# Kernel tuning notes

Measured on AMD Instinct MI355X. Metric: run time of the kernel, lower is better.

The kernel has to match this reference:

```python
import jax, jax.numpy as jnp
import numpy as np

N_NODES = 100000
N_EDGES = 800000
D_IN = 128      # input_dim (node feature dim)
D_HID = 128     # output_dim (MLP hidden dim)


def setup_inputs() -> dict:
    key = jax.random.key(0)
    ks = jax.random.split(key, 7)
    node_emb = jax.random.normal(ks[0], (N_NODES, D_IN), dtype=jnp.float32)
    src = jax.random.randint(ks[1], (N_EDGES,), 0, N_NODES, dtype=jnp.int64)
    dst = jax.random.randint(ks[2], (N_EDGES,), 0, N_NODES, dtype=jnp.int64)
    W1 = jax.random.normal(ks[3], (2 * D_IN, D_HID), dtype=jnp.float32) / np.sqrt(2 * D_IN)
    b1 = jnp.zeros((D_HID,), dtype=jnp.float32)
    W2 = jax.random.normal(ks[4], (D_HID, 1), dtype=jnp.float32) / np.sqrt(D_HID)
    b2 = jnp.zeros((1,), dtype=jnp.float32)
    u_gate = jax.random.uniform(ks[5], (N_EDGES, 1), dtype=jnp.float32)  # torch.rand noise for gumbel gate
    u_bern = jax.random.uniform(ks[6], (N_EDGES,), dtype=jnp.float32)    # uniform noise for RelaxedBernoulli.rsample
    return {"node_emb": node_emb, "src": src, "dst": dst,
            "W1": W1, "b1": b1, "W2": W2, "b2": b2,
            "u_gate": u_gate, "u_bern": u_bern}


def reference(node_emb, src, dst, W1, b1, W2, b2, u_gate, u_bern):
    BIAS = 1e-4          # bias in forward
    TEMP_GATE = 1.0      # temperature in forward
    TEMP_BERN = 0.9      # temperature passed to build_prob_neighbourhood

    # edge gather + concat: [E, 2*D_IN]
    edge_emb = jnp.concatenate([node_emb[src], node_emb[dst]], axis=1)
    # 2-layer per-edge MLP -> logits [E, 1]
    h = jax.nn.relu(edge_emb @ W1 + b1)
    edge_logits = h @ W2 + b2

    # gumbel-sigmoid gate: eps in (BIAS, 1-BIAS]
    eps = (BIAS - (1.0 - BIAS)) * u_gate + (1.0 - BIAS)
    gate_inputs = (jnp.log(eps) - jnp.log1p(-eps) + edge_logits) / TEMP_GATE
    edge_weight = jax.nn.sigmoid(gate_inputs).squeeze(-1)  # [E]

    # build_prob_neighbourhood: RelaxedBernoulli(temperature=0.9, probs=clamped).rsample()
    attention = jnp.clip(edge_weight, 0.01, 0.99)
    bern_logits = jnp.log(attention) - jnp.log1p(-attention)
    u = jnp.clip(u_bern, 1e-7, 1.0 - 1e-7)
    w = jax.nn.sigmoid((bern_logits + jnp.log(u) - jnp.log1p(-u)) / TEMP_BERN)

    # mask = (w > 0).detach().float(); w = w*mask + 0*(1-mask)
    mask = jax.lax.stop_gradient((w > 0.0).astype(w.dtype))
    return w * mask
```

## Files before the change

### kernel.cpp

```cpp
#include <hip/hip_runtime.h>
#include <hip/hip_bf16.h>
#include <cstdint>

#define D  128
#define NT 256

typedef __attribute__((ext_vector_type(8))) short bf16x8;
typedef __attribute__((ext_vector_type(4))) float f32x4;

__device__ __forceinline__ unsigned int packbf(float lo, float hi) {
    const unsigned int ulo = __float_as_uint(lo) + 0x8000u;
    const unsigned int uhi = __float_as_uint(hi) + 0x8000u;
    return __builtin_amdgcn_perm(uhi, ulo, 0x07060302);
}

__global__ __launch_bounds__(256, 2) void node_mlp_mfma(
    const float* __restrict__ x, const float* __restrict__ W1,
    unsigned short* __restrict__ T, int N)
{
    const int lane = threadIdx.x & 63;
    const int wid  = (blockIdx.x * blockDim.x + threadIdx.x) >> 6;
    const int half = wid & 1;
    const int strip = wid >> 1;
    const int lr = lane & 15;
    const int lg = lane >> 4;

    const int NCH = (N + 15) >> 4;

    bf16x8 wf[8][4];
    #pragma unroll
    for (int cg = 0; cg < 8; ++cg) {
        #pragma unroll
        for (int ks = 0; ks < 4; ++ks) {
            const int k0 = (half ? 128 : 0) + 32 * ks + 8 * lg;
            const float* wp = W1 + (size_t)k0 * D + cg * 16 + lr;
            float l0 = wp[0*D], l1 = wp[1*D], l2 = wp[2*D], l3 = wp[3*D];
            float l4 = wp[4*D], l5 = wp[5*D], l6 = wp[6*D], l7 = wp[7*D];
            uint4 u;
            u.x = packbf(l0, l1); u.y = packbf(l2, l3);
            u.z = packbf(l4, l5); u.w = packbf(l6, l7);
            wf[cg][ks] = __builtin_bit_cast(bf16x8, u);
        }
    }

    int c = strip;
    if (c >= NCH) return;

    size_t row = (size_t)(c * 16 + lr);
    if (row > (size_t)(N - 1)) row = (size_t)(N - 1);
    const float4* pf = reinterpret_cast<const float4*>(x + row * D + 8 * lg);
    float4 r0 = pf[0],  r1 = pf[1],  r2 = pf[8],  r3 = pf[9];
    float4 r4 = pf[16], r5 = pf[17], r6 = pf[24], r7 = pf[25];

    while (c < NCH) {
        bf16x8 xf[4];
        {
            uint4 u;
            u.x = packbf(r0.x, r0.y); u.y = packbf(r0.z, r0.w);
            u.z = packbf(r1.x, r1.y); u.w = packbf(r1.z, r1.w);
            xf[0] = __builtin_bit_cast(bf16x8, u);
            u.x = packbf(r2.x, r2.y); u.y = packbf(r2.z, r2.w);
            u.z = packbf(r3.x, r3.y); u.w = packbf(r3.z, r3.w);
            xf[1] = __builtin_bit_cast(bf16x8, u);
            u.x = packbf(r4.x, r4.y); u.y = packbf(r4.z, r4.w);
            u.z = packbf(r5.x, r5.y); u.w = packbf(r5.z, r5.w);
            xf[2] = __builtin_bit_cast(bf16x8, u);
            u.x = packbf(r6.x, r6.y); u.y = packbf(r6.z, r6.w);
            u.z = packbf(r7.x, r7.y); u.w = packbf(r7.z, r7.w);
            xf[3] = __builtin_bit_cast(bf16x8, u);
        }

        const int cn = c + 1024;
        {
            size_t row2 = (size_t)(cn * 16 + lr);
            if (row2 > (size_t)(N - 1)) row2 = (size_t)(N - 1);
            pf = reinterpret_cast<const float4*>(x + row2 * D + 8 * lg);
        }
        float4 t0 = pf[0],  t1 = pf[1],  t2 = pf[8],  t3 = pf[9];
        float4 t4 = pf[16], t5 = pf[17], t6 = pf[24], t7 = pf[25];

        f32x4 acc[8];
        #pragma unroll
        for (int cg = 0; cg < 8; ++cg) acc[cg] = (f32x4){0.f, 0.f, 0.f, 0.f};
        #pragma unroll
        for (int ks = 0; ks < 4; ++ks) {
            #pragma unroll
            for (int cg = 0; cg < 8; ++cg) {
                acc[cg] = __builtin_amdgcn_mfma_f32_16x16x32_bf16(
                    wf[cg][ks], xf[ks], acc[cg], 0, 0, 0);
            }
        }

        const int node = c * 16 + lr;
        if (node < N) {
            unsigned short* orow = T + (size_t)node * NT + half * 128 + lg * 4;
            #pragma unroll
            for (int cg = 0; cg < 8; ++cg) {
                uint2 o;
                o.x = packbf(acc[cg][0], acc[cg][1]);
                o.y = packbf(acc[cg][2], acc[cg][3]);
                *reinterpret_cast<uint2*>(orow + cg * 16) = o;
            }
        }

        r0 = t0; r1 = t1; r2 = t2; r3 = t3;
        r4 = t4; r5 = t5; r6 = t6; r7 = t7;
        c = cn;
    }
}

__device__ __forceinline__ float acc_pair(uint32_t wa, uint32_t wb,
                                          float blo, float bhi,
                                          float w2lo, float w2hi, float p) {
    const float alo = __uint_as_float(wa << 16);
    const float ahi = __uint_as_float(wa & 0xffff0000u);
    const float clo = __uint_as_float(wb << 16);
    const float chi = __uint_as_float(wb & 0xffff0000u);
    const float h0 = fmaxf(alo + clo + blo, 0.f);
    const float h1 = fmaxf(ahi + chi + bhi, 0.f);
    p = fmaf(h0, w2lo, p);
    p = fmaf(h1, w2hi, p);
    return p;
}

__global__ __launch_bounds__(256) void edge_kernel(
    const unsigned short* __restrict__ T,
    const int* __restrict__ src, const int* __restrict__ dst,
    const float* __restrict__ b1, const float* __restrict__ W2,
    const float* __restrict__ b2,
    const float* __restrict__ u_gate, const float* __restrict__ u_bern,
    float* __restrict__ out, int E)
{
    const int gid = blockIdx.x * blockDim.x + threadIdx.x;
    const int e = gid >> 3;
    if (e >= E) return;
    const int sub = threadIdx.x & 7;

    const int s = src[e];
    const int d = dst[e];

    const uint4* Ap = reinterpret_cast<const uint4*>(T + (size_t)s * NT + sub * 16);
    const uint4* Bp = reinterpret_cast<const uint4*>(T + (size_t)d * NT + 128 + sub * 16);
    const float4* Bv = reinterpret_cast<const float4*>(b1 + sub * 16);
    const float4* Wv = reinterpret_cast<const float4*>(W2 + sub * 16);

    const uint4 a0 = Ap[0], a1 = Ap[1];
    const uint4 c0 = Bp[0], c1 = Bp[1];
    const float4 bb0 = Bv[0], bb1 = Bv[1], bb2 = Bv[2], bb3 = Bv[3];
    const float4 w0 = Wv[0], w1 = Wv[1], w2 = Wv[2], w3 = Wv[3];

    float p = 0.f;
    p = acc_pair(a0.x, c0.x, bb0.x, bb0.y, w0.x, w0.y, p);
    p = acc_pair(a0.y, c0.y, bb0.z, bb0.w, w0.z, w0.w, p);
    p = acc_pair(a0.z, c0.z, bb1.x, bb1.y, w1.x, w1.y, p);
    p = acc_pair(a0.w, c0.w, bb1.z, bb1.w, w1.z, w1.w, p);
    p = acc_pair(a1.x, c1.x, bb2.x, bb2.y, w2.x, w2.y, p);
    p = acc_pair(a1.y, c1.y, bb2.z, bb2.w, w2.z, w2.w, p);
    p = acc_pair(a1.z, c1.z, bb3.x, bb3.y, w3.x, w3.y, p);
    p = acc_pair(a1.w, c1.w, bb3.z, bb3.w, w3.z, w3.w, p);

    p += __shfl_xor(p, 1, 64);
    p += __shfl_xor(p, 2, 64);
    p += __shfl_xor(p, 4, 64);

    if (sub == 0) {
        const float logit = p + b2[0];

        const float ug  = u_gate[e];
        const float eps = fmaf(-0.9998f, ug, 0.9999f);
        const float g   = logf(eps) - log1pf(-eps) + logit;
        const float ew  = 1.f / (1.f + expf(-g));

        const float att = fminf(fmaxf(ew, 0.01f), 0.99f);
        const float bl  = logf(att) - log1pf(-att);
        const float ub  = fminf(fmaxf(u_bern[e], 1e-7f), 1.f - 1e-7f);
        const float arg = (bl + logf(ub) - log1pf(-ub)) * (1.0f / 0.9f);
        const float wv  = 1.f / (1.f + expf(-arg));

        out[e] = wv;
    }
}

extern "C" void kernel_launch(void* const* d_in, const int* in_sizes, int n_in,
                              void* d_out, int out_size, void* d_ws, size_t ws_size,
                              hipStream_t stream)
{
    const float* node_emb = (const float*)d_in[0];
    const int*   src      = (const int*)d_in[1];
    const int*   dst      = (const int*)d_in[2];
    const float* W1       = (const float*)d_in[3];
    const float* b1       = (const float*)d_in[4];
    const float* W2       = (const float*)d_in[5];
    const float* b2       = (const float*)d_in[6];
    const float* u_gate   = (const float*)d_in[7];
    const float* u_bern   = (const float*)d_in[8];
    float* out = (float*)d_out;

    const int N = in_sizes[0] / D;
    const int E = in_sizes[1];

    unsigned short* T = (unsigned short*)d_ws;

    node_mlp_mfma<<<512, 256, 0, stream>>>(node_emb, W1, T, N);

    const long long dotThreads = (long long)E * 8;
    const int blocksE = (int)((dotThreads + 255) / 256);
    edge_kernel<<<blocksE, 256, 0, stream>>>(T, src, dst, b1, W2, b2,
                                             u_gate, u_bern, out, E);
}
```

Baseline: 200.3 us.

## Pre-pack W1 into LDS, compute both halves per wave, persistent prefetching edge kernel

```diff
diff --git a/kernel.cpp b/kernel.cpp
--- a/kernel.cpp
+++ b/kernel.cpp
@@ -14,45 +14,57 @@
     return __builtin_amdgcn_perm(uhi, ulo, 0x07060302);
 }
 
-__global__ __launch_bounds__(256, 2) void node_mlp_mfma(
-    const float* __restrict__ x, const float* __restrict__ W1,
+__global__ __launch_bounds__(256) void pack_w1(
+    const float* __restrict__ W1, unsigned short* __restrict__ Wp)
+{
+    const int t = blockIdx.x * 256 + threadIdx.x;
+    if (t >= 4096) return;
+    const int lane = t & 63;
+    const int fc = t >> 6;
+    const int cg = fc >> 2, ks = fc & 3;
+    const int lr = lane & 15, lg = lane >> 4;
+    const int half = cg >> 3;
+    const int col = (cg & 7) * 16 + lr;
+    const int krow = half * 128 + ks * 32 + lg * 8;
+    const float* wp = W1 + (size_t)krow * D + col;
+    uint4 u;
+    u.x = packbf(wp[0 * D], wp[1 * D]);
+    u.y = packbf(wp[2 * D], wp[3 * D]);
+    u.z = packbf(wp[4 * D], wp[5 * D]);
+    u.w = packbf(wp[6 * D], wp[7 * D]);
+    reinterpret_cast<uint4*>(Wp)[t] = u;
+}
+
+__global__ __launch_bounds__(512, 4) void node_mlp_mfma(
+    const float* __restrict__ x, const unsigned short* __restrict__ Wp,
     unsigned short* __restrict__ T, int N)
 {
+    __shared__ uint4 ldsW[4096];
+
+    {
+        const uint4* s = reinterpret_cast<const uint4*>(Wp);
+        #pragma unroll
+        for (int i = 0; i < 8; ++i)
+            ldsW[threadIdx.x + i * 512] = s[threadIdx.x + i * 512];
+    }
+    __syncthreads();
+
     const int lane = threadIdx.x & 63;
-    const int wid  = (blockIdx.x * blockDim.x + threadIdx.x) >> 6;
-    const int half = wid & 1;
-    const int strip = wid >> 1;
-    const int lr = lane & 15;
-    const int lg = lane >> 4;
-
+    const int wib  = threadIdx.x >> 6;
+    const int wid  = blockIdx.x * 8 + wib;
+    const int nW   = gridDim.x * 8;
+    const int lr = lane & 15, lg = lane >> 4;
     const int NCH = (N + 15) >> 4;
 
-    bf16x8 wf[8][4];
-    #pragma unroll
-    for (int cg = 0; cg < 8; ++cg) {
-        #pragma unroll
-        for (int ks = 0; ks < 4; ++ks) {
-            const int k0 = (half ? 128 : 0) + 32 * ks + 8 * lg;
-            const float* wp = W1 + (size_t)k0 * D + cg * 16 + lr;
-            float l0 = wp[0*D], l1 = wp[1*D], l2 = wp[2*D], l3 = wp[3*D];
-            float l4 = wp[4*D], l5 = wp[5*D], l6 = wp[6*D], l7 = wp[7*D];
-            uint4 u;
-            u.x = packbf(l0, l1); u.y = packbf(l2, l3);
-            u.z = packbf(l4, l5); u.w = packbf(l6, l7);
-            wf[cg][ks] = __builtin_bit_cast(bf16x8, u);
-        }
-    }
-
-    int c = strip;
-    if (c >= NCH) return;
-
-    size_t row = (size_t)(c * 16 + lr);
-    if (row > (size_t)(N - 1)) row = (size_t)(N - 1);
-    const float4* pf = reinterpret_cast<const float4*>(x + row * D + 8 * lg);
-    float4 r0 = pf[0],  r1 = pf[1],  r2 = pf[8],  r3 = pf[9];
-    float4 r4 = pf[16], r5 = pf[17], r6 = pf[24], r7 = pf[25];
-
-    while (c < NCH) {
+    const uint4* fragBase = ldsW + lane;
+
+    for (int c = wid; c < NCH; c += nW) {
+        int row = c * 16 + lr;
+        if (row >= N) row = N - 1;
+        const float4* pf = reinterpret_cast<const float4*>(x + (size_t)row * D + 8 * lg);
+        const float4 r0 = pf[0],  r1 = pf[1],  r2 = pf[8],  r3 = pf[9];
+        const float4 r4 = pf[16], r5 = pf[17], r6 = pf[24], r7 = pf[25];
+
         bf16x8 xf[4];
         {
             uint4 u;
@@ -70,42 +82,30 @@
             xf[3] = __builtin_bit_cast(bf16x8, u);
         }
 
-        const int cn = c + 1024;
-        {
-            size_t row2 = (size_t)(cn * 16 + lr);
-            if (row2 > (size_t)(N - 1)) row2 = (size_t)(N - 1);
-            pf = reinterpret_cast<const float4*>(x + row2 * D + 8 * lg);
-        }
-        float4 t0 = pf[0],  t1 = pf[1],  t2 = pf[8],  t3 = pf[9];
-        float4 t4 = pf[16], t5 = pf[17], t6 = pf[24], t7 = pf[25];
-
-        f32x4 acc[8];
+        f32x4 acc[16];
         #pragma unroll
-        for (int cg = 0; cg < 8; ++cg) acc[cg] = (f32x4){0.f, 0.f, 0.f, 0.f};
+        for (int cg = 0; cg < 16; ++cg) acc[cg] = (f32x4){0.f, 0.f, 0.f, 0.f};
+
         #pragma unroll
         for (int ks = 0; ks < 4; ++ks) {
             #pragma unroll
-            for (int cg = 0; cg < 8; ++cg) {
-                acc[cg] = __builtin_amdgcn_mfma_f32_16x16x32_bf16(
-                    wf[cg][ks], xf[ks], acc[cg], 0, 0, 0);
+            for (int cg = 0; cg < 16; ++cg) {
+                const bf16x8 wf = __builtin_bit_cast(bf16x8, fragBase[(cg * 4 + ks) * 64]);
+                acc[cg] = __builtin_amdgcn_mfma_f32_16x16x32_bf16(wf, xf[ks], acc[cg], 0, 0, 0);
             }
         }
 
         const int node = c * 16 + lr;
         if (node < N) {
-            unsigned short* orow = T + (size_t)node * NT + half * 128 + lg * 4;
+            unsigned short* orow = T + (size_t)node * NT + lg * 4;
             #pragma unroll
-            for (int cg = 0; cg < 8; ++cg) {
+            for (int cg = 0; cg < 16; ++cg) {
                 uint2 o;
                 o.x = packbf(acc[cg][0], acc[cg][1]);
                 o.y = packbf(acc[cg][2], acc[cg][3]);
                 *reinterpret_cast<uint2*>(orow + cg * 16) = o;
             }
         }
-
-        r0 = t0; r1 = t1; r2 = t2; r3 = t3;
-        r4 = t4; r5 = t5; r6 = t6; r7 = t7;
-        c = cn;
     }
 }
 
@@ -131,53 +131,68 @@
     const float* __restrict__ u_gate, const float* __restrict__ u_bern,
     float* __restrict__ out, int E)
 {
-    const int gid = blockIdx.x * blockDim.x + threadIdx.x;
-    const int e = gid >> 3;
+    const int sub = threadIdx.x & 7;
+    const int g0 = (blockIdx.x * blockDim.x + threadIdx.x) >> 3;
+    const int gstride = (gridDim.x * blockDim.x) >> 3;
+
+    const float4* Bv = reinterpret_cast<const float4*>(b1 + sub * 16);
+    const float4* Wv = reinterpret_cast<const float4*>(W2 + sub * 16);
+    const float4 bb0 = Bv[0], bb1 = Bv[1], bb2 = Bv[2], bb3 = Bv[3];
+    const float4 w0 = Wv[0], w1 = Wv[1], w2 = Wv[2], w3 = Wv[3];
+    const float b2v = b2[0];
+
+    int e = g0;
     if (e >= E) return;
-    const int sub = threadIdx.x & 7;
-
-    const int s = src[e];
-    const int d = dst[e];
-
+
+    int s = src[e], d = dst[e];
     const uint4* Ap = reinterpret_cast<const uint4*>(T + (size_t)s * NT + sub * 16);
     const uint4* Bp = reinterpret_cast<const uint4*>(T + (size_t)d * NT + 128 + sub * 16);
-    const float4* Bv = reinterpret_cast<const float4*>(b1 + sub * 16);
-    const float4* Wv = reinterpret_cast<const float4*>(W2 + sub * 16);
-
-    const uint4 a0 = Ap[0], a1 = Ap[1];
-    const uint4 c0 = Bp[0], c1 = Bp[1];
-    const float4 bb0 = Bv[0], bb1 = Bv[1], bb2 = Bv[2], bb3 = Bv[3];
-    const float4 w0 = Wv[0], w1 = Wv[1], w2 = Wv[2], w3 = Wv[3];
-
-    float p = 0.f;
-    p = acc_pair(a0.x, c0.x, bb0.x, bb0.y, w0.x, w0.y, p);
-    p = acc_pair(a0.y, c0.y, bb0.z, bb0.w, w0.z, w0.w, p);
-    p = acc_pair(a0.z, c0.z, bb1.x, bb1.y, w1.x, w1.y, p);
-    p = acc_pair(a0.w, c0.w, bb1.z, bb1.w, w1.z, w1.w, p);
-    p = acc_pair(a1.x, c1.x, bb2.x, bb2.y, w2.x, w2.y, p);
-    p = acc_pair(a1.y, c1.y, bb2.z, bb2.w, w2.z, w2.w, p);
-    p = acc_pair(a1.z, c1.z, bb3.x, bb3.y, w3.x, w3.y, p);
-    p = acc_pair(a1.w, c1.w, bb3.z, bb3.w, w3.z, w3.w, p);
-
-    p += __shfl_xor(p, 1, 64);
-    p += __shfl_xor(p, 2, 64);
-    p += __shfl_xor(p, 4, 64);
-
-    if (sub == 0) {
-        const float logit = p + b2[0];
-
-        const float ug  = u_gate[e];
-        const float eps = fmaf(-0.9998f, ug, 0.9999f);
-        const float g   = logf(eps) - log1pf(-eps) + logit;
-        const float ew  = 1.f / (1.f + expf(-g));
-
-        const float att = fminf(fmaxf(ew, 0.01f), 0.99f);
-        const float bl  = logf(att) - log1pf(-att);
-        const float ub  = fminf(fmaxf(u_bern[e], 1e-7f), 1.f - 1e-7f);
-        const float arg = (bl + logf(ub) - log1pf(-ub)) * (1.0f / 0.9f);
-        const float wv  = 1.f / (1.f + expf(-arg));
-
-        out[e] = wv;
+    uint4 a0 = Ap[0], a1 = Ap[1];
+    uint4 c0 = Bp[0], c1 = Bp[1];
+
+    for (;;) {
+        const int en = e + gstride;
+        const bool more = en < E;
+        uint4 na0, na1, nc0, nc1;
+        if (more) {
+            const int sn = src[en], dn = dst[en];
+            const uint4* An = reinterpret_cast<const uint4*>(T + (size_t)sn * NT + sub * 16);
+            const uint4* Bn = reinterpret_cast<const uint4*>(T + (size_t)dn * NT + 128 + sub * 16);
+            na0 = An[0]; na1 = An[1];
+            nc0 = Bn[0]; nc1 = Bn[1];
+        }
+
+        float p = 0.f;
+        p = acc_pair(a0.x, c0.x, bb0.x, bb0.y, w0.x, w0.y, p);
+        p = acc_pair(a0.y, c0.y, bb0.z, bb0.w, w0.z, w0.w, p);
+        p = acc_pair(a0.z, c0.z, bb1.x, bb1.y, w1.x, w1.y, p);
+        p = acc_pair(a0.w, c0.w, bb1.z, bb1.w, w1.z, w1.w, p);
+        p = acc_pair(a1.x, c1.x, bb2.x, bb2.y, w2.x, w2.y, p);
+        p = acc_pair(a1.y, c1.y, bb2.z, bb2.w, w2.z, w2.w, p);
+        p = acc_pair(a1.z, c1.z, bb3.x, bb3.y, w3.x, w3.y, p);
+        p = acc_pair(a1.w, c1.w, bb3.z, bb3.w, w3.z, w3.w, p);
+
+        p += __shfl_xor(p, 1, 64);
+        p += __shfl_xor(p, 2, 64);
+        p += __shfl_xor(p, 4, 64);
+
+        if (sub == 0) {
+            const float logit = p + b2v;
+            const float ug  = u_gate[e];
+            const float eps = fmaf(-0.9998f, ug, 0.9999f);
+            const float g   = logf(eps) - log1pf(-eps) + logit;
+            const float ew  = 1.f / (1.f + expf(-g));
+            const float att = fminf(fmaxf(ew, 0.01f), 0.99f);
+            const float bl  = logf(att) - log1pf(-att);
+            const float ub  = fminf(fmaxf(u_bern[e], 1e-7f), 1.f - 1e-7f);
+            const float arg = (bl + logf(ub) - log1pf(-ub)) * (1.0f / 0.9f);
+            const float wv  = 1.f / (1.f + expf(-arg));
+            out[e] = wv;
+        }
+
+        if (!more) break;
+        a0 = na0; a1 = na1; c0 = nc0; c1 = nc1;
+        e = en;
     }
 }
 
@@ -199,12 +214,11 @@
     const int N = in_sizes[0] / D;
     const int E = in_sizes[1];
 
-    unsigned short* T = (unsigned short*)d_ws;
-
-    node_mlp_mfma<<<512, 256, 0, stream>>>(node_emb, W1, T, N);
-
-    const long long dotThreads = (long long)E * 8;
-    const int blocksE = (int)((dotThreads + 255) / 256);
-    edge_kernel<<<blocksE, 256, 0, stream>>>(T, src, dst, b1, W2, b2,
-                                             u_gate, u_bern, out, E);
-}
+    unsigned short* Wp = (unsigned short*)d_ws;
+    unsigned short* T  = Wp + 32768;
+
+    pack_w1<<<16, 256, 0, stream>>>(W1, Wp);
+    node_mlp_mfma<<<512, 512, 0, stream>>>(node_emb, Wp, T, N);
+    edge_kernel<<<1024, 256, 0, stream>>>(T, src, dst, b1, W2, b2,
+                                          u_gate, u_bern, out, E);
+}
```

Result: slower. 382.7 us (+91.1%).
